# Optimization experiments

Hardware: AMD Instinct MI355X
Metric: run time of the kernel (lower is better)

The kernel has to match this reference:

```python
import jax, jax.numpy as jnp
import numpy as np

H = 512  # hidden_size
A = 1.0  # hard_sigm slope


def hard_sigm(a, x):
    return jnp.clip((a * x + 1.0) / 2.0, 0.0, 1.0)


def setup_inputs() -> dict:
    key = jax.random.key(0)
    ks = jax.random.split(key, 10)
    B = 8192
    bottom, top = 512, 512
    stdv = 1.0 / np.sqrt(H)
    u = lambda k, shp: jax.random.uniform(k, shp, jnp.float32, -stdv, stdv)
    return {
        "c": jax.random.normal(ks[0], (H, B), jnp.float32),
        "h_bottom": jax.random.normal(ks[1], (bottom, B), jnp.float32),
        "h": jax.random.normal(ks[2], (H, B), jnp.float32),
        "h_top": jax.random.normal(ks[3], (top, B), jnp.float32),
        "z": jax.random.uniform(ks[4], (1, B), jnp.float32),
        "z_bottom": jax.random.uniform(ks[5], (1, B), jnp.float32),
        "U_11": u(ks[6], (4 * H + 1, H)),
        "U_21": u(ks[7], (4 * H + 1, top)),
        "W_01": u(ks[8], (4 * H + 1, bottom)),
        "bias": u(ks[9], (4 * H + 1,)),
    }


def reference(c, h_bottom, h, h_top, z, z_bottom, U_11, U_21, W_01, bias):
    # z, z_bottom: (1, B) boundary indicators broadcast over the gate axis
    s_recur = (1.0 - z) * (U_11 @ h)          # (4H+1, B)
    s_topdown = z * (U_21 @ h_top)            # last_layer=False
    s_bottomup = z_bottom * (W_01 @ h_bottom)
    f_s = s_recur + s_topdown + s_bottomup + bias[:, None]

    f = jax.nn.sigmoid(f_s[0:H, :])
    i = jax.nn.sigmoid(f_s[H:2 * H, :])
    o = jax.nn.sigmoid(f_s[2 * H:3 * H, :])
    g = jnp.tanh(f_s[3 * H:4 * H, :])
    z_hat = hard_sigm(A, f_s[4 * H:4 * H + 1, :])  # (1, B)

    ig = i * g
    c_new = z * ig + (1.0 - z) * (1.0 - z_bottom) * c \
        + (1.0 - z) * z_bottom * (f * c + ig)
    tanh_c = jnp.tanh(c_new)
    h_new = z * o * tanh_c + (1.0 - z) * (1.0 - z_bottom) * h \
        + (1.0 - z) * z_bottom * o * tanh_c
    return (h_new, c_new, z_hat)
```

## Files before the change

kernel.cpp:

```cpp
#include <hip/hip_runtime.h>
#include <hip/hip_bf16.h>

#define HH 512
#define BB 8192
#define KK 1536
#define NT 48
#define HB 4194304
#define BLOB 8192

typedef __bf16 bhalf;
typedef __bf16 bf16x8 __attribute__((ext_vector_type(8)));
typedef float  f32x4  __attribute__((ext_vector_type(4)));

typedef __attribute__((address_space(1))) void* as1_t;
typedef __attribute__((address_space(3))) void* as3_t;

#define GLDS(src, dst) __builtin_amdgcn_global_load_lds((as1_t)(void*)(src), (as3_t)(void*)(dst), 16, 0, 0)
#define SBAR() asm volatile("s_barrier" ::: "memory")
#define VM0()  asm volatile("s_waitcnt vmcnt(0)" ::: "memory")


__global__ __launch_bounds__(256) void prep_x(
    const float* __restrict__ h, const float* __restrict__ ht,
    const float* __restrict__ hb, const float* __restrict__ z,
    const float* __restrict__ zb, bhalf* __restrict__ XtP)
{
    __shared__ float tile[32][257];
    const int tid = threadIdx.x;
    const int kt  = blockIdx.x;
    const int nt  = blockIdx.y;
    const int n   = nt * 256 + tid;
    const int kb  = kt * 32;

    const float* src; int kr; float scale;
    if (kb < 512)       { src = h;  kr = kb;        scale = 1.f - z[n]; }
    else if (kb < 1024) { src = ht; kr = kb - 512;  scale = z[n]; }
    else                { src = hb; kr = kb - 1024; scale = zb[n]; }

    #pragma unroll
    for (int kk = 0; kk < 32; ++kk)
        tile[kk][tid] = src[(size_t)(kr + kk) * BB + n] * scale;
    __syncthreads();

    bhalf* blob = XtP + (size_t)(nt * NT + kt) * BLOB;
    #pragma unroll
    for (int q = 0; q < 4; ++q) {
        const int s  = q * 256 + tid;
        const int rb = s >> 6, w = s & 63;
        const int hh = w >> 4, lrr = w & 15;
        const int nloc = rb * 16 + lrr, kloc = hh * 8;
        bf16x8 r;
        #pragma unroll
        for (int e = 0; e < 8; ++e) r[e] = (bhalf)tile[kloc + e][nloc];
        *(bf16x8*)(blob + s * 8) = r;
    }
}

__global__ __launch_bounds__(256) void prep_w(
    const float* __restrict__ U11, const float* __restrict__ U21,
    const float* __restrict__ W01, bhalf* __restrict__ WcP)
{
    const int o    = blockIdx.x * 4 + (threadIdx.x >> 6);
    const int lane = threadIdx.x & 63;
    const int g = o >> 9, j = o & 511;
    const int mp = 4 * j + g;
    const int mt = mp >> 8, rb = (mp >> 4) & 15, lrr = mp & 15;

    #pragma unroll
    for (int p = 0; p < 3; ++p) {
        const float* src = (p == 0) ? U11 : (p == 1) ? U21 : W01;
        const float* rp  = src + (size_t)o * 512 + lane * 8;
        float4 v0 = *(const float4*)rp;
        float4 v1 = *(const float4*)(rp + 4);
        bf16x8 r;
        r[0]=(bhalf)v0.x; r[1]=(bhalf)v0.y; r[2]=(bhalf)v0.z; r[3]=(bhalf)v0.w;
        r[4]=(bhalf)v1.x; r[5]=(bhalf)v1.y; r[6]=(bhalf)v1.z; r[7]=(bhalf)v1.w;
        const int kt = p * 16 + (lane >> 2);
        const int hh = lane & 3;
        *(bf16x8*)(WcP + (size_t)(mt * NT + kt) * BLOB
                   + rb * 512 + hh * 128 + lrr * 8) = r;
    }
}

__device__ __forceinline__ float sigmf(float x)    { return 1.f / (1.f + __expf(-x)); }
__device__ __forceinline__ float tanhfast(float x) { return 2.f / (1.f + __expf(-2.f * x)) - 1.f; }

__global__ __launch_bounds__(512, 4) void gemm_fused(
    const bhalf* __restrict__ WcP, const bhalf* __restrict__ XtP,
    const float* __restrict__ bias, const float* __restrict__ c_in,
    const float* __restrict__ h_in, const float* __restrict__ z,
    const float* __restrict__ zb, const float* __restrict__ U11,
    const float* __restrict__ U21, const float* __restrict__ W01,
    float* __restrict__ out)
{
    __shared__ bhalf As[2][BLOB];
    __shared__ bhalf Bs[2][BLOB / 2];

    const int tid  = threadIdx.x;
    const int lane = tid & 63;
    const int wid  = tid >> 6;
    const int wm   = wid >> 1, wn = wid & 1;
    const int lr   = lane & 15, hi = lane >> 4;
    const int soff = hi * 128 + lr * 8;

    const int xcd = blockIdx.x & 7;
    const int i   = blockIdx.x >> 3;
    const int mt  = ((xcd & 3) << 1) | (i & 1);
    const int nt2 = ((xcd >> 2) << 5) | (i >> 1);
    const int n0 = nt2 * 128;
    const int jb = mt * 64;

    const bhalf* gA = WcP + (size_t)mt * (NT * BLOB) + tid * 8;
    const bhalf* gB = XtP + (size_t)(nt2 >> 1) * (NT * BLOB)
                          + (nt2 & 1) * (BLOB / 2) + tid * 8;

    const bhalf* pA0 = &As[0][wm * 2048 + soff];
    const bhalf* pA1 = &As[1][wm * 2048 + soff];
    const bhalf* pB0 = &Bs[0][wn * 2048 + soff];
    const bhalf* pB1 = &Bs[1][wn * 2048 + soff];

    const float* wU = U11 + (size_t)2048 * 512;
    const float* wV = U21 + (size_t)2048 * 512;
    const float* wW = W01 + (size_t)2048 * 512;
    const int hh8 = ((tid >> 4) & 3) * 8;
    float zacc = 0.f;

#define STAGE(t, bf) do {                                                     \
        const bhalf* sa_ = gA + (size_t)(t) * BLOB;                           \
        const bhalf* sb_ = gB + (size_t)(t) * BLOB;                           \
        GLDS(sa_,        &As[bf][tid * 8]);                                   \
        GLDS(sa_ + 4096, &As[bf][tid * 8 + 4096]);                            \
        GLDS(sb_,        &Bs[bf][tid * 8]);                                   \
    } while (0)

#define MF(mi, ni, A_, B_) acc[mi][ni] = \
    __builtin_amdgcn_mfma_f32_16x16x32_bf16(A_, B_, acc[mi][ni], 0, 0, 0)

#define CT(q) do {                                                            \
    bf16x8 b0 = *(const bf16x8*)(pB##q);                                      \
    bf16x8 b1 = *(const bf16x8*)(pB##q + 512);                                \
    bf16x8 b2 = *(const bf16x8*)(pB##q + 1024);                               \
    bf16x8 b3 = *(const bf16x8*)(pB##q + 1536);                               \
    bf16x8 a0 = *(const bf16x8*)(pA##q);                                      \
    bf16x8 a1 = *(const bf16x8*)(pA##q + 512);                                \
    bf16x8 a2 = *(const bf16x8*)(pA##q + 1024);                               \
    bf16x8 a3 = *(const bf16x8*)(pA##q + 1536);                               \
    __builtin_amdgcn_s_setprio(1);                                            \
    MF(0,0,a0,b0); MF(0,1,a0,b1); MF(0,2,a0,b2); MF(0,3,a0,b3);               \
    MF(1,0,a1,b0); MF(1,1,a1,b1); MF(1,2,a1,b2); MF(1,3,a1,b3);               \
    MF(2,0,a2,b0); MF(2,1,a2,b1); MF(2,2,a2,b2); MF(2,3,a2,b3);               \
    MF(3,0,a3,b0); MF(3,1,a3,b1); MF(3,2,a3,b2); MF(3,3,a3,b3);               \
    __builtin_amdgcn_s_setprio(0);                                            \
} while (0)

#define ZACC(q, t_) do { if (mt == 0) {                                       \
    const float* ws_ = ((t_) < 16) ? wU + (t_) * 32                           \
                     : ((t_) < 32) ? wV + ((t_) - 16) * 32                    \
                     : wW + ((t_) - 32) * 32;                                 \
    float4 w0_ = *(const float4*)(ws_ + hh8);                                 \
    float4 w1_ = *(const float4*)(ws_ + hh8 + 4);                             \
    bf16x8 xv_ = *(const bf16x8*)(&Bs[q][tid * 8]);                           \
    zacc += (float)xv_[0]*w0_.x + (float)xv_[1]*w0_.y + (float)xv_[2]*w0_.z   \
          + (float)xv_[3]*w0_.w + (float)xv_[4]*w1_.x + (float)xv_[5]*w1_.y   \
          + (float)xv_[6]*w1_.z + (float)xv_[7]*w1_.w;                        \
} } while (0)

    f32x4 acc[4][4] = {};

    STAGE(0, 0);

    for (int t = 0; t < 46; t += 2) {
        VM0(); SBAR(); STAGE(t + 1, 1); ZACC(0, t);     CT(0);
        VM0(); SBAR(); STAGE(t + 2, 0); ZACC(1, t + 1); CT(1);
    }
    VM0(); SBAR(); STAGE(47, 1); ZACC(0, 46); CT(0);
    VM0(); SBAR();               ZACC(1, 47); CT(1);

    if (mt == 0) {
        __syncthreads();
        float* zs = (float*)&Bs[0][0];
        zs[tid] = zacc;
        __syncthreads();
        if (tid < 128) {
            const int base = (tid >> 4) * 64 + (tid & 15);
            const float s = zs[base] + zs[base + 16]
                          + zs[base + 32] + zs[base + 48];
            const float v = (s + bias[2048] + 1.f) * 0.5f;
            out[(size_t)2 * HB + n0 + tid] = fminf(fmaxf(v, 0.f), 1.f);
        }
    }

    const int colbase = n0 + wn * 64 + lr;
    const int jloc0   = wm * 16 + hi;
    float zc[4], zbc[4];
    #pragma unroll
    for (int ni = 0; ni < 4; ++ni) {
        zc[ni]  = z[colbase + ni * 16];
        zbc[ni] = zb[colbase + ni * 16];
    }
    #pragma unroll
    for (int mi = 0; mi < 4; ++mi) {
        const int j = jb + jloc0 + mi * 4;
        const float bf_ = bias[j];
        const float bi_ = bias[512 + j];
        const float bo_ = bias[1024 + j];
        const float bg_ = bias[1536 + j];
        #pragma unroll
        for (int ni = 0; ni < 4; ++ni) {
            const int col = colbase + ni * 16;
            const size_t idx = (size_t)j * BB + col;
            const float cv = c_in[idx];
            const float hv = h_in[idx];
            const float fv = sigmf(acc[mi][ni][0] + bf_);
            const float iv = sigmf(acc[mi][ni][1] + bi_);
            const float ov = sigmf(acc[mi][ni][2] + bo_);
            const float gv = tanhfast(acc[mi][ni][3] + bg_);
            const float ig = iv * gv;
            const float zq = zc[ni], zbq = zbc[ni];
            const float cn = zq * ig + (1.f - zq) * (1.f - zbq) * cv
                           + (1.f - zq) * zbq * (fv * cv + ig);
            const float tc = tanhfast(cn);
            const float hn = (zq + (1.f - zq) * zbq) * ov * tc
                           + (1.f - zq) * (1.f - zbq) * hv;
            out[idx]      = hn;
            out[HB + idx] = cn;
        }
    }
}

extern "C" void kernel_launch(void* const* d_in, const int* in_sizes, int n_in,
                              void* d_out, int out_size, void* d_ws, size_t ws_size,
                              hipStream_t stream) {
    const float* c    = (const float*)d_in[0];
    const float* hb   = (const float*)d_in[1];
    const float* h    = (const float*)d_in[2];
    const float* ht   = (const float*)d_in[3];
    const float* z    = (const float*)d_in[4];
    const float* zb   = (const float*)d_in[5];
    const float* U11  = (const float*)d_in[6];
    const float* U21  = (const float*)d_in[7];
    const float* W01  = (const float*)d_in[8];
    const float* bias = (const float*)d_in[9];
    float* out = (float*)d_out;

    char* ws = (char*)d_ws;
    bhalf* XtP = (bhalf*)ws;
    bhalf* WcP = (bhalf*)(ws + 25165824);

    prep_x    <<<dim3(48, 32), 256, 0, stream>>>(h, ht, hb, z, zb, XtP);
    prep_w    <<<512, 256, 0, stream>>>(U11, U21, W01, WcP);
    gemm_fused<<<512, 512, 0, stream>>>(WcP, XtP, bias, c, h, z, zb,
                                        U11, U21, W01, out);
}
```

Before: 82.96 us.

## Merge prep kernels and move z_hat row dot-product into the prep pass

Fuses prep_x and prep_w into a single launch and computes the z_hat gate row's partial dot products in fp32 during the activation prep, writing 48 per-k-tile partials to workspace. The GEMM kernel no longer runs the per-iteration ZACC work in the mt==0 blocks. Those blocks instead sum the 48 partials once before the main loop. This removes load imbalance and extra LDS/global reads from the hot loop and saves one launch, at the cost of an extra 1.5 MB partial buffer write and read. It also changes z_hat to use unrounded fp32 inputs.

```diff
diff --git a/kernel.cpp b/kernel.cpp
--- a/kernel.cpp
+++ b/kernel.cpp
@@ -20,65 +20,75 @@
 #define VM0()  asm volatile("s_waitcnt vmcnt(0)" ::: "memory")
 
 
-__global__ __launch_bounds__(256) void prep_x(
+__global__ __launch_bounds__(256) void prep_all(
     const float* __restrict__ h, const float* __restrict__ ht,
     const float* __restrict__ hb, const float* __restrict__ z,
-    const float* __restrict__ zb, bhalf* __restrict__ XtP)
+    const float* __restrict__ zb, const float* __restrict__ U11,
+    const float* __restrict__ U21, const float* __restrict__ W01,
+    bhalf* __restrict__ XtP, bhalf* __restrict__ WcP,
+    float* __restrict__ zpart)
 {
-    __shared__ float tile[32][257];
     const int tid = threadIdx.x;
-    const int kt  = blockIdx.x;
-    const int nt  = blockIdx.y;
-    const int n   = nt * 256 + tid;
-    const int kb  = kt * 32;
-
-    const float* src; int kr; float scale;
-    if (kb < 512)       { src = h;  kr = kb;        scale = 1.f - z[n]; }
-    else if (kb < 1024) { src = ht; kr = kb - 512;  scale = z[n]; }
-    else                { src = hb; kr = kb - 1024; scale = zb[n]; }
-
-    #pragma unroll
-    for (int kk = 0; kk < 32; ++kk)
-        tile[kk][tid] = src[(size_t)(kr + kk) * BB + n] * scale;
-    __syncthreads();
-
-    bhalf* blob = XtP + (size_t)(nt * NT + kt) * BLOB;
-    #pragma unroll
-    for (int q = 0; q < 4; ++q) {
-        const int s  = q * 256 + tid;
-        const int rb = s >> 6, w = s & 63;
-        const int hh = w >> 4, lrr = w & 15;
-        const int nloc = rb * 16 + lrr, kloc = hh * 8;
-        bf16x8 r;
-        #pragma unroll
-        for (int e = 0; e < 8; ++e) r[e] = (bhalf)tile[kloc + e][nloc];
-        *(bf16x8*)(blob + s * 8) = r;
-    }
-}
-
-__global__ __launch_bounds__(256) void prep_w(
-    const float* __restrict__ U11, const float* __restrict__ U21,
-    const float* __restrict__ W01, bhalf* __restrict__ WcP)
-{
-    const int o    = blockIdx.x * 4 + (threadIdx.x >> 6);
-    const int lane = threadIdx.x & 63;
-    const int g = o >> 9, j = o & 511;
-    const int mp = 4 * j + g;
-    const int mt = mp >> 8, rb = (mp >> 4) & 15, lrr = mp & 15;
-
-    #pragma unroll
-    for (int p = 0; p < 3; ++p) {
-        const float* src = (p == 0) ? U11 : (p == 1) ? U21 : W01;
-        const float* rp  = src + (size_t)o * 512 + lane * 8;
-        float4 v0 = *(const float4*)rp;
-        float4 v1 = *(const float4*)(rp + 4);
-        bf16x8 r;
-        r[0]=(bhalf)v0.x; r[1]=(bhalf)v0.y; r[2]=(bhalf)v0.z; r[3]=(bhalf)v0.w;
-        r[4]=(bhalf)v1.x; r[5]=(bhalf)v1.y; r[6]=(bhalf)v1.z; r[7]=(bhalf)v1.w;
-        const int kt = p * 16 + (lane >> 2);
-        const int hh = lane & 3;
-        *(bf16x8*)(WcP + (size_t)(mt * NT + kt) * BLOB
-                   + rb * 512 + hh * 128 + lrr * 8) = r;
+    const int b   = blockIdx.x;
+
+    if (b < 1536) {
+        __shared__ float tile[32][257];
+        const int kt = b % 48;
+        const int nt = b / 48;
+        const int n  = nt * 256 + tid;
+        const int kb = kt * 32;
+
+        const float* src; const float* wsrc; int kr; float scale;
+        if (kb < 512)       { src = h;  wsrc = U11 + (size_t)2048 * 512 + kb;
+                              kr = kb;        scale = 1.f - z[n]; }
+        else if (kb < 1024) { src = ht; wsrc = U21 + (size_t)2048 * 512 + (kb - 512);
+                              kr = kb - 512;  scale = z[n]; }
+        else                { src = hb; wsrc = W01 + (size_t)2048 * 512 + (kb - 1024);
+                              kr = kb - 1024; scale = zb[n]; }
+
+        float zp = 0.f;
+        #pragma unroll
+        for (int kk = 0; kk < 32; ++kk) {
+            const float v = src[(size_t)(kr + kk) * BB + n] * scale;
+            tile[kk][tid] = v;
+            zp += v * wsrc[kk];
+        }
+        zpart[(size_t)kt * BB + n] = zp;
+        __syncthreads();
+
+        bhalf* blob = XtP + (size_t)(nt * NT + kt) * BLOB;
+        #pragma unroll
+        for (int q = 0; q < 4; ++q) {
+            const int s  = q * 256 + tid;
+            const int rb = s >> 6, w = s & 63;
+            const int hh = w >> 4, lrr = w & 15;
+            const int nloc = rb * 16 + lrr, kloc = hh * 8;
+            bf16x8 r;
+            #pragma unroll
+            for (int e = 0; e < 8; ++e) r[e] = (bhalf)tile[kloc + e][nloc];
+            *(bf16x8*)(blob + s * 8) = r;
+        }
+    } else {
+        const int o    = (b - 1536) * 4 + (tid >> 6);
+        const int lane = tid & 63;
+        const int g = o >> 9, j = o & 511;
+        const int mp = 4 * j + g;
+        const int mt = mp >> 8, rb = (mp >> 4) & 15, lrr = mp & 15;
+
+        #pragma unroll
+        for (int p = 0; p < 3; ++p) {
+            const float* src = (p == 0) ? U11 : (p == 1) ? U21 : W01;
+            const float* rp  = src + (size_t)o * 512 + lane * 8;
+            float4 v0 = *(const float4*)rp;
+            float4 v1 = *(const float4*)(rp + 4);
+            bf16x8 r;
+            r[0]=(bhalf)v0.x; r[1]=(bhalf)v0.y; r[2]=(bhalf)v0.z; r[3]=(bhalf)v0.w;
+            r[4]=(bhalf)v1.x; r[5]=(bhalf)v1.y; r[6]=(bhalf)v1.z; r[7]=(bhalf)v1.w;
+            const int kt = p * 16 + (lane >> 2);
+            const int hh = lane & 3;
+            *(bf16x8*)(WcP + (size_t)(mt * NT + kt) * BLOB
+                       + rb * 512 + hh * 128 + lrr * 8) = r;
+        }
     }
 }
 
@@ -89,8 +99,7 @@
     const bhalf* __restrict__ WcP, const bhalf* __restrict__ XtP,
     const float* __restrict__ bias, const float* __restrict__ c_in,
     const float* __restrict__ h_in, const float* __restrict__ z,
-    const float* __restrict__ zb, const float* __restrict__ U11,
-    const float* __restrict__ U21, const float* __restrict__ W01,
+    const float* __restrict__ zb, const float* __restrict__ zpart,
     float* __restrict__ out)
 {
     __shared__ bhalf As[2][BLOB];
@@ -118,12 +127,6 @@
     const bhalf* pA1 = &As[1][wm * 2048 + soff];
     const bhalf* pB0 = &Bs[0][wn * 2048 + soff];
     const bhalf* pB1 = &Bs[1][wn * 2048 + soff];
-
-    const float* wU = U11 + (size_t)2048 * 512;
-    const float* wV = U21 + (size_t)2048 * 512;
-    const float* wW = W01 + (size_t)2048 * 512;
-    const int hh8 = ((tid >> 4) & 3) * 8;
-    float zacc = 0.f;
 
 #define STAGE(t, bf) do {                                                     \
         const bhalf* sa_ = gA + (size_t)(t) * BLOB;                           \
@@ -153,42 +156,25 @@
     __builtin_amdgcn_s_setprio(0);                                            \
 } while (0)
 
-#define ZACC(q, t_) do { if (mt == 0) {                                       \
-    const float* ws_ = ((t_) < 16) ? wU + (t_) * 32                           \
-                     : ((t_) < 32) ? wV + ((t_) - 16) * 32                    \
-                     : wW + ((t_) - 32) * 32;                                 \
-    float4 w0_ = *(const float4*)(ws_ + hh8);                                 \
-    float4 w1_ = *(const float4*)(ws_ + hh8 + 4);                             \
-    bf16x8 xv_ = *(const bf16x8*)(&Bs[q][tid * 8]);                           \
-    zacc += (float)xv_[0]*w0_.x + (float)xv_[1]*w0_.y + (float)xv_[2]*w0_.z   \
-          + (float)xv_[3]*w0_.w + (float)xv_[4]*w1_.x + (float)xv_[5]*w1_.y   \
-          + (float)xv_[6]*w1_.z + (float)xv_[7]*w1_.w;                        \
-} } while (0)
-
     f32x4 acc[4][4] = {};
 
     STAGE(0, 0);
 
+    if (mt == 0 && tid < 128) {
+        const int n = n0 + tid;
+        float s = 0.f;
+        #pragma unroll
+        for (int kt2 = 0; kt2 < NT; ++kt2) s += zpart[(size_t)kt2 * BB + n];
+        const float v = (s + bias[2048] + 1.f) * 0.5f;
+        out[(size_t)2 * HB + n] = fminf(fmaxf(v, 0.f), 1.f);
+    }
+
     for (int t = 0; t < 46; t += 2) {
-        VM0(); SBAR(); STAGE(t + 1, 1); ZACC(0, t);     CT(0);
-        VM0(); SBAR(); STAGE(t + 2, 0); ZACC(1, t + 1); CT(1);
-    }
-    VM0(); SBAR(); STAGE(47, 1); ZACC(0, 46); CT(0);
-    VM0(); SBAR();               ZACC(1, 47); CT(1);
-
-    if (mt == 0) {
-        __syncthreads();
-        float* zs = (float*)&Bs[0][0];
-        zs[tid] = zacc;
-        __syncthreads();
-        if (tid < 128) {
-            const int base = (tid >> 4) * 64 + (tid & 15);
-            const float s = zs[base] + zs[base + 16]
-                          + zs[base + 32] + zs[base + 48];
-            const float v = (s + bias[2048] + 1.f) * 0.5f;
-            out[(size_t)2 * HB + n0 + tid] = fminf(fmaxf(v, 0.f), 1.f);
-        }
-    }
+        VM0(); SBAR(); STAGE(t + 1, 1); CT(0);
+        VM0(); SBAR(); STAGE(t + 2, 0); CT(1);
+    }
+    VM0(); SBAR(); STAGE(47, 1); CT(0);
+    VM0(); SBAR(); CT(1);
 
     const int colbase = n0 + wn * 64 + lr;
     const int jloc0   = wm * 16 + hi;
@@ -244,11 +230,12 @@
     float* out = (float*)d_out;
 
     char* ws = (char*)d_ws;
-    bhalf* XtP = (bhalf*)ws;
-    bhalf* WcP = (bhalf*)(ws + 25165824);
-
-    prep_x    <<<dim3(48, 32), 256, 0, stream>>>(h, ht, hb, z, zb, XtP);
-    prep_w    <<<512, 256, 0, stream>>>(U11, U21, W01, WcP);
+    bhalf* XtP   = (bhalf*)ws;
+    bhalf* WcP   = (bhalf*)(ws + 25165824);
+    float* zpart = (float*)(ws + 25165824 + 6291456);
+
+    prep_all  <<<2048, 256, 0, stream>>>(h, ht, hb, z, zb, U11, U21, W01,
+                                         XtP, WcP, zpart);
     gemm_fused<<<512, 512, 0, stream>>>(WcP, XtP, bias, c, h, z, zb,
-                                        U11, U21, W01, out);
+                                        zpart, out);
 }
```

New measurement: 74.44 us (median of 2 runs). 10.3% less time.
